# Performance work log

Hardware: AMD Instinct MI355X
Metric: run time of the kernel (lower is better)

Reference implementation:

```python
import jax, jax.numpy as jnp
import numpy as np


def setup_inputs() -> dict:
    key = jax.random.key(0)
    k1, k2 = jax.random.split(key)
    pred_corners = jax.random.normal(k1, (2048, 8, 3), dtype=jnp.float32)
    gt_corners = jax.random.normal(k2, (2048, 8, 3), dtype=jnp.float32)
    return {"pred_corners": pred_corners, "gt_corners": gt_corners}


def _chamfer(pred_corners, gt_corners):
    # flatten boxes -> point clouds: [Np*8, 3], [Ng*8, 3]
    x = pred_corners.reshape(-1, 3)
    y = gt_corners.reshape(-1, 3)
    x2 = jnp.sum(x * x, axis=-1)  # [N]
    y2 = jnp.sum(y * y, axis=-1)  # [M]
    d2 = x2[:, None] + y2[None, :] - 2.0 * jnp.einsum("nd,md->nm", x, y)
    dist = jnp.sqrt(jnp.maximum(d2, 0.0))  # [N, M]
    # bidirectional min, averaged per box (8 corners) then over boxes
    min_p2g = jnp.min(dist, axis=1).reshape(-1, 8).mean(axis=1)
    min_g2p = jnp.min(dist, axis=0).reshape(-1, 8).mean(axis=1)
    return min_p2g.mean() + min_g2p.mean()


def reference(pred_corners, gt_corners):
    return _chamfer(pred_corners, gt_corners)
```

## Files before the change

### kernel.cpp

```cpp
#include <hip/hip_runtime.h>


#define NPTS   16384
#define BLOCK  256
#define XW     128
#define XCH    512
#define NXB    (NPTS / XCH)
#define YRNG   1024
#define NYR    (NPTS / YRNG)
#define CHT    8
#define NCH    (YRNG / (CHT * 16))
#define ONEBF  0x3F80

#define WS_PPB  (1u << 20)
#define WS_PGA  (2u << 20)
#define WS_PGB  (3u << 20)
#define WS_PART (4u << 20)

typedef __attribute__((ext_vector_type(8))) short bf16x8;
typedef __attribute__((ext_vector_type(4))) float f32x4;
typedef __attribute__((ext_vector_type(4))) unsigned int u32x4;

__device__ inline unsigned short f2bf(float f) {
    unsigned int u = __float_as_uint(f);
    return (unsigned short)((u + 0x7FFFu + ((u >> 16) & 1u)) >> 16);
}
__device__ inline float bf2f(unsigned short h) {
    return __uint_as_float((unsigned int)h << 16);
}
__device__ inline void split3(float v, unsigned short* s) {
    unsigned short h = f2bf(v);  float r = v - bf2f(h);
    unsigned short m = f2bf(r);  r -= bf2f(m);
    s[0] = h; s[1] = m; s[2] = f2bf(r);
}

__device__ inline void build_rows(const float p[3], unsigned short* a,
                                  unsigned short* b) {
    const int CI[6] = {0, 0, 1, 0, 1, 2};
    const int CJ[6] = {0, 1, 0, 2, 1, 0};
    unsigned short xs[3][3], nn[3], t[3];
#pragma unroll
    for (int d = 0; d < 3; ++d) {
        split3(p[d], t);
        xs[0][d] = t[0]; xs[1][d] = t[1]; xs[2][d] = t[2];
    }
    split3(-0.5f * (p[0]*p[0] + p[1]*p[1] + p[2]*p[2]), nn);
#pragma unroll
    for (int c = 0; c < 6; ++c)
#pragma unroll
        for (int d = 0; d < 3; ++d) {
            a[c*3+d] = xs[CI[c]][d];
            b[c*3+d] = xs[CJ[c]][d];
        }
#pragma unroll
    for (int k = 0; k < 3; ++k) {
        a[18+k] = nn[k];  b[18+k] = ONEBF;
        a[21+k] = ONEBF;  b[21+k] = nn[k];
    }
#pragma unroll
    for (int k = 24; k < 32; ++k) { a[k] = 0; b[k] = 0; }
}

__device__ inline void store_row_swz(uint4* dst4, int i, const unsigned short* s) {
    unsigned int w[16];
#pragma unroll
    for (int k = 0; k < 16; ++k)
        w[k] = (unsigned int)s[2*k] | ((unsigned int)s[2*k+1] << 16);
    const int base = (i >> 4) * 64 + (i & 15);
#pragma unroll
    for (int kgc = 0; kgc < 4; ++kgc)
        dst4[base + kgc * 16] = make_uint4(w[4*kgc], w[4*kgc+1],
                                           w[4*kgc+2], w[4*kgc+3]);
}

__global__ __launch_bounds__(256) void pack_points(
        const float* __restrict__ pred, const float* __restrict__ gt,
        unsigned short* __restrict__ Ppa, unsigned short* __restrict__ Ppb,
        unsigned short* __restrict__ Pga, unsigned short* __restrict__ Pgb,
        float* __restrict__ out) {
    const int i = blockIdx.x * 256 + threadIdx.x;
    if (i == 0) out[0] = 0.0f;
    if (i >= NPTS) return;
    float p[3] = {pred[3*i], pred[3*i+1], pred[3*i+2]};
    float q[3] = {gt[3*i],   gt[3*i+1],   gt[3*i+2]};
    unsigned short ra[32], rb[32];
    build_rows(p, ra, rb);
    store_row_swz(reinterpret_cast<uint4*>(Ppa), i, ra);
    store_row_swz(reinterpret_cast<uint4*>(Ppb), i, rb);
    build_rows(q, ra, rb);
    store_row_swz(reinterpret_cast<uint4*>(Pga), i, ra);
    store_row_swz(reinterpret_cast<uint4*>(Pgb), i, rb);
}

template <int CTRL>
__device__ inline float rormax(float v) {
    int t = __builtin_amdgcn_update_dpp(0, __float_as_int(v), CTRL, 0xF, 0xF,
                                        false);
    return fmaxf(v, __int_as_float(t));
}

__global__ __launch_bounds__(BLOCK, 1) void chamfer_rowmin(
        const unsigned short* __restrict__ Ppa,
        const unsigned short* __restrict__ Ppb,
        const unsigned short* __restrict__ Pga,
        const unsigned short* __restrict__ Pgb,
        float* __restrict__ part) {
    const int xb  = blockIdx.x;
    const int yr  = blockIdx.y;
    const int dir = blockIdx.z;
    const unsigned short* __restrict__ Ap = dir ? Pga : Ppa;
    const unsigned short* __restrict__ Bp = dir ? Ppb : Pgb;
    const int tid = threadIdx.x;
    const int lane = tid & 63, w = tid >> 6;
    const int col = lane & 15, kg = lane >> 4;
    const int frag = kg * 16 + col;

    __shared__ uint4 buf[2][CHT * 64];
    __shared__ float rowacc[XCH];

    const uint4* ap = reinterpret_cast<const uint4*>(Ap);
    const int tile0 = xb * 32 + w * 8;
    u32x4 af[8];
#pragma unroll
    for (int xi = 0; xi < 8; ++xi)
        af[xi] = *reinterpret_cast<const u32x4*>(&ap[(tile0 + xi) * 64 + frag]);

    f32x4 rmax[8];
#pragma unroll
    for (int xi = 0; xi < 8; ++xi)
        rmax[xi] = (f32x4){-3.0e38f, -3.0e38f, -3.0e38f, -3.0e38f};

    const u32x4 zz = {0u, 0u, 0u, 0u};

    const uint4* bp = reinterpret_cast<const uint4*>(Bp) + (size_t)(yr * 64) * 64;
    uint4 s0 = bp[tid];
    uint4 s1 = bp[256 + tid];

#pragma unroll 1
    for (int c = 0; c < NCH; ++c) {
        buf[c & 1][tid]       = s0;
        buf[c & 1][256 + tid] = s1;
        __syncthreads();
        if (c + 1 < NCH) {
            s0 = bp[(c + 1) * 512 + tid];
            s1 = bp[(c + 1) * 512 + 256 + tid];
        }
        const uint4* bb = buf[c & 1];
#pragma unroll
        for (int t = 0; t < CHT; t += 2) {
            u32x4 c0 = *reinterpret_cast<const u32x4*>(&bb[(t + 0) * 64 + frag]);
            u32x4 c1 = *reinterpret_cast<const u32x4*>(&bb[(t + 1) * 64 + frag]);
#pragma unroll
            for (int xi = 0; xi < 8; ++xi) {
                f32x4 A, B;
                asm("s_nop 1\n\t"
                    "v_mfma_f32_16x16x32_bf16 %0, %2, %3, %5\n\t"
                    "v_mfma_f32_16x16x32_bf16 %1, %2, %4, %5\n\t"
                    "s_nop 7\n\t"
                    "s_nop 7\n\t"
                    "s_nop 3"
                    : "=&v"(A), "=&v"(B)
                    : "v"(af[xi]), "v"(c0), "v"(c1), "v"(zz));
                rmax[xi].x = fmaxf(fmaxf(A.x, B.x), rmax[xi].x);
                rmax[xi].y = fmaxf(fmaxf(A.y, B.y), rmax[xi].y);
                rmax[xi].z = fmaxf(fmaxf(A.z, B.z), rmax[xi].z);
                rmax[xi].w = fmaxf(fmaxf(A.w, B.w), rmax[xi].w);
            }
        }
        __syncthreads();
    }

#pragma unroll
    for (int xi = 0; xi < 8; ++xi) {
#pragma unroll
        for (int cc = 0; cc < 4; ++cc) {
            float v = rmax[xi][cc];
            v = rormax<0x121>(v);
            v = rormax<0x122>(v);
            v = rormax<0x124>(v);
            v = rormax<0x128>(v);
            if (col == 0)
                rowacc[w * XW + xi * 16 + kg * 4 + cc] = fmaxf(-2.0f * v, 0.0f);
        }
    }
    __syncthreads();
    float* dst = part + (size_t)(dir * NYR + yr) * NPTS + xb * XCH;
    dst[tid]       = rowacc[tid];
    dst[256 + tid] = rowacc[256 + tid];
}

__global__ __launch_bounds__(256) void chamfer_reduce(
        const float* __restrict__ part, float* __restrict__ out) {
    const int gid = blockIdx.x * 256 + threadIdx.x;
    const int side = gid >> 12;
    const int idx4 = (gid & 4095) * 4;
    const float* base = part + (size_t)side * NYR * NPTS + idx4;
    float4 m = make_float4(3.0e38f, 3.0e38f, 3.0e38f, 3.0e38f);
#pragma unroll
    for (int c = 0; c < NYR; ++c) {
        float4 v = *reinterpret_cast<const float4*>(base + (size_t)c * NPTS);
        m.x = fminf(m.x, v.x); m.y = fminf(m.y, v.y);
        m.z = fminf(m.z, v.z); m.w = fminf(m.w, v.w);
    }
    float s = sqrtf(m.x) + sqrtf(m.y) + sqrtf(m.z) + sqrtf(m.w);
#pragma unroll
    for (int o = 32; o > 0; o >>= 1)
        s += __shfl_down(s, o, 64);
    if ((threadIdx.x & 63) == 0)
        atomicAdd(out, s * (1.0f / (float)NPTS));
}

extern "C" void kernel_launch(void* const* d_in, const int* in_sizes, int n_in,
                              void* d_out, int out_size, void* d_ws, size_t ws_size,
                              hipStream_t stream) {
    const float* pred = (const float*)d_in[0];
    const float* gt   = (const float*)d_in[1];
    float* out        = (float*)d_out;
    unsigned short* Ppa = (unsigned short*)d_ws;
    unsigned short* Ppb = (unsigned short*)((char*)d_ws + WS_PPB);
    unsigned short* Pga = (unsigned short*)((char*)d_ws + WS_PGA);
    unsigned short* Pgb = (unsigned short*)((char*)d_ws + WS_PGB);
    float* part         = (float*)((char*)d_ws + WS_PART);

    hipLaunchKernelGGL(pack_points, dim3(NPTS / 256), dim3(256), 0, stream,
                       pred, gt, Ppa, Ppb, Pga, Pgb, out);
    hipLaunchKernelGGL(chamfer_rowmin, dim3(NXB, NYR, 2), dim3(BLOCK), 0, stream,
                       Ppa, Ppb, Pga, Pgb, part);
    hipLaunchKernelGGL(chamfer_reduce, dim3(2 * NPTS / 1024), dim3(256), 0, stream,
                       part, out);
}
```

Measured before the change: 90.13 us.

## Compute both chamfer directions from one distance matrix pass

Replaces the two-direction launch, which computed the pred-to-gt and gt-to-pred matrices separately, with one kernel that computes each distance tile once. Row minima come from the existing per-row max path, and column minima are built by reducing across the MFMA output and lanes into shared memory. This roughly halves the MFMA work and packs only two of the four operand arrays. The y-range per block is cut to 512 to keep the grid large, and the hand-scheduled inline asm with its s_nop padding is replaced by compiler builtins. The cost is extra fmax and shuffle work per tile, plus more shared memory and partial-result traffic per block.

```diff
diff --git a/kernel.cpp b/kernel.cpp
--- a/kernel.cpp
+++ b/kernel.cpp
@@ -6,20 +6,19 @@
 #define XW     128
 #define XCH    512
 #define NXB    (NPTS / XCH)
-#define YRNG   1024
+#define YRNG   512
 #define NYR    (NPTS / YRNG)
 #define CHT    8
 #define NCH    (YRNG / (CHT * 16))
 #define ONEBF  0x3F80
 
-#define WS_PPB  (1u << 20)
-#define WS_PGA  (2u << 20)
-#define WS_PGB  (3u << 20)
-#define WS_PART (4u << 20)
+#define WS_PGB  (1u << 20)
+#define WS_PART (2u << 20)
+#define NROWSL  NYR
+#define NCOLSL  NXB
 
 typedef __attribute__((ext_vector_type(8))) short bf16x8;
 typedef __attribute__((ext_vector_type(4))) float f32x4;
-typedef __attribute__((ext_vector_type(4))) unsigned int u32x4;
 
 __device__ inline unsigned short f2bf(float f) {
     unsigned int u = __float_as_uint(f);
@@ -75,8 +74,7 @@
 
 __global__ __launch_bounds__(256) void pack_points(
         const float* __restrict__ pred, const float* __restrict__ gt,
-        unsigned short* __restrict__ Ppa, unsigned short* __restrict__ Ppb,
-        unsigned short* __restrict__ Pga, unsigned short* __restrict__ Pgb,
+        unsigned short* __restrict__ Ppa, unsigned short* __restrict__ Pgb,
         float* __restrict__ out) {
     const int i = blockIdx.x * 256 + threadIdx.x;
     if (i == 0) out[0] = 0.0f;
@@ -86,9 +84,7 @@
     unsigned short ra[32], rb[32];
     build_rows(p, ra, rb);
     store_row_swz(reinterpret_cast<uint4*>(Ppa), i, ra);
-    store_row_swz(reinterpret_cast<uint4*>(Ppb), i, rb);
     build_rows(q, ra, rb);
-    store_row_swz(reinterpret_cast<uint4*>(Pga), i, ra);
     store_row_swz(reinterpret_cast<uint4*>(Pgb), i, rb);
 }
 
@@ -99,17 +95,12 @@
     return fmaxf(v, __int_as_float(t));
 }
 
-__global__ __launch_bounds__(BLOCK, 1) void chamfer_rowmin(
+__global__ __launch_bounds__(BLOCK, 1) void chamfer_bidi(
         const unsigned short* __restrict__ Ppa,
-        const unsigned short* __restrict__ Ppb,
-        const unsigned short* __restrict__ Pga,
         const unsigned short* __restrict__ Pgb,
         float* __restrict__ part) {
-    const int xb  = blockIdx.x;
-    const int yr  = blockIdx.y;
-    const int dir = blockIdx.z;
-    const unsigned short* __restrict__ Ap = dir ? Pga : Ppa;
-    const unsigned short* __restrict__ Bp = dir ? Ppb : Pgb;
+    const int yr = blockIdx.x;
+    const int xb = blockIdx.y;
     const int tid = threadIdx.x;
     const int lane = tid & 63, w = tid >> 6;
     const int col = lane & 15, kg = lane >> 4;
@@ -117,22 +108,26 @@
 
     __shared__ uint4 buf[2][CHT * 64];
     __shared__ float rowacc[XCH];
-
-    const uint4* ap = reinterpret_cast<const uint4*>(Ap);
+    __shared__ float colacc[4][YRNG];
+
+    const uint4* ap = reinterpret_cast<const uint4*>(Ppa);
     const int tile0 = xb * 32 + w * 8;
-    u32x4 af[8];
+    bf16x8 af[8];
 #pragma unroll
     for (int xi = 0; xi < 8; ++xi)
-        af[xi] = *reinterpret_cast<const u32x4*>(&ap[(tile0 + xi) * 64 + frag]);
+        af[xi] = *reinterpret_cast<const bf16x8*>(&ap[(tile0 + xi) * 64 + frag]);
 
     f32x4 rmax[8];
 #pragma unroll
     for (int xi = 0; xi < 8; ++xi)
         rmax[xi] = (f32x4){-3.0e38f, -3.0e38f, -3.0e38f, -3.0e38f};
-
-    const u32x4 zz = {0u, 0u, 0u, 0u};
-
-    const uint4* bp = reinterpret_cast<const uint4*>(Bp) + (size_t)(yr * 64) * 64;
+    float cmax[CHT];
+#pragma unroll
+    for (int yt = 0; yt < CHT; ++yt) cmax[yt] = -3.0e38f;
+
+    const f32x4 z4 = {0.0f, 0.0f, 0.0f, 0.0f};
+
+    const uint4* bp = reinterpret_cast<const uint4*>(Pgb) + (size_t)yr * 2048;
     uint4 s0 = bp[tid];
     uint4 s1 = bp[256 + tid];
 
@@ -148,24 +143,29 @@
         const uint4* bb = buf[c & 1];
 #pragma unroll
         for (int t = 0; t < CHT; t += 2) {
-            u32x4 c0 = *reinterpret_cast<const u32x4*>(&bb[(t + 0) * 64 + frag]);
-            u32x4 c1 = *reinterpret_cast<const u32x4*>(&bb[(t + 1) * 64 + frag]);
+            bf16x8 b0 = *reinterpret_cast<const bf16x8*>(&bb[(t + 0) * 64 + frag]);
+            bf16x8 b1 = *reinterpret_cast<const bf16x8*>(&bb[(t + 1) * 64 + frag]);
 #pragma unroll
             for (int xi = 0; xi < 8; ++xi) {
-                f32x4 A, B;
-                asm("s_nop 1\n\t"
-                    "v_mfma_f32_16x16x32_bf16 %0, %2, %3, %5\n\t"
-                    "v_mfma_f32_16x16x32_bf16 %1, %2, %4, %5\n\t"
-                    "s_nop 7\n\t"
-                    "s_nop 7\n\t"
-                    "s_nop 3"
-                    : "=&v"(A), "=&v"(B)
-                    : "v"(af[xi]), "v"(c0), "v"(c1), "v"(zz));
+                f32x4 A = __builtin_amdgcn_mfma_f32_16x16x32_bf16(af[xi], b0, z4, 0, 0, 0);
+                f32x4 B = __builtin_amdgcn_mfma_f32_16x16x32_bf16(af[xi], b1, z4, 0, 0, 0);
                 rmax[xi].x = fmaxf(fmaxf(A.x, B.x), rmax[xi].x);
                 rmax[xi].y = fmaxf(fmaxf(A.y, B.y), rmax[xi].y);
                 rmax[xi].z = fmaxf(fmaxf(A.z, B.z), rmax[xi].z);
                 rmax[xi].w = fmaxf(fmaxf(A.w, B.w), rmax[xi].w);
+                float ta = fmaxf(fmaxf(A.x, A.y), A.z);
+                cmax[t]     = fmaxf(fmaxf(ta, A.w), cmax[t]);
+                float tb = fmaxf(fmaxf(B.x, B.y), B.z);
+                cmax[t + 1] = fmaxf(fmaxf(tb, B.w), cmax[t + 1]);
             }
+        }
+#pragma unroll
+        for (int yt = 0; yt < CHT; ++yt) {
+            float v = cmax[yt];
+            v = fmaxf(v, __shfl_xor(v, 16, 64));
+            v = fmaxf(v, __shfl_xor(v, 32, 64));
+            if (kg == 0) colacc[w][c * 128 + yt * 16 + col] = v;
+            cmax[yt] = -3.0e38f;
         }
         __syncthreads();
     }
@@ -184,9 +184,18 @@
         }
     }
     __syncthreads();
-    float* dst = part + (size_t)(dir * NYR + yr) * NPTS + xb * XCH;
-    dst[tid]       = rowacc[tid];
-    dst[256 + tid] = rowacc[256 + tid];
+
+    float* rdst = part + (size_t)yr * NPTS + xb * XCH;
+    rdst[tid]       = rowacc[tid];
+    rdst[256 + tid] = rowacc[256 + tid];
+    float* cdst = part + (size_t)(NROWSL + xb) * NPTS + yr * YRNG;
+#pragma unroll
+    for (int j = 0; j < 2; ++j) {
+        int idx = j * 256 + tid;
+        float v = fmaxf(fmaxf(colacc[0][idx], colacc[1][idx]),
+                        fmaxf(colacc[2][idx], colacc[3][idx]));
+        cdst[idx] = fmaxf(-2.0f * v, 0.0f);
+    }
 }
 
 __global__ __launch_bounds__(256) void chamfer_reduce(
@@ -194,10 +203,10 @@
     const int gid = blockIdx.x * 256 + threadIdx.x;
     const int side = gid >> 12;
     const int idx4 = (gid & 4095) * 4;
-    const float* base = part + (size_t)side * NYR * NPTS + idx4;
+    const float* base = part + (size_t)side * NROWSL * NPTS + idx4;
     float4 m = make_float4(3.0e38f, 3.0e38f, 3.0e38f, 3.0e38f);
 #pragma unroll
-    for (int c = 0; c < NYR; ++c) {
+    for (int c = 0; c < 32; ++c) {
         float4 v = *reinterpret_cast<const float4*>(base + (size_t)c * NPTS);
         m.x = fminf(m.x, v.x); m.y = fminf(m.y, v.y);
         m.z = fminf(m.z, v.z); m.w = fminf(m.w, v.w);
@@ -217,15 +226,13 @@
     const float* gt   = (const float*)d_in[1];
     float* out        = (float*)d_out;
     unsigned short* Ppa = (unsigned short*)d_ws;
-    unsigned short* Ppb = (unsigned short*)((char*)d_ws + WS_PPB);
-    unsigned short* Pga = (unsigned short*)((char*)d_ws + WS_PGA);
     unsigned short* Pgb = (unsigned short*)((char*)d_ws + WS_PGB);
     float* part         = (float*)((char*)d_ws + WS_PART);
 
     hipLaunchKernelGGL(pack_points, dim3(NPTS / 256), dim3(256), 0, stream,
-                       pred, gt, Ppa, Ppb, Pga, Pgb, out);
-    hipLaunchKernelGGL(chamfer_rowmin, dim3(NXB, NYR, 2), dim3(BLOCK), 0, stream,
-                       Ppa, Ppb, Pga, Pgb, part);
+                       pred, gt, Ppa, Pgb, out);
+    hipLaunchKernelGGL(chamfer_bidi, dim3(NYR, NXB), dim3(BLOCK), 0, stream,
+                       Ppa, Pgb, part);
     hipLaunchKernelGGL(chamfer_reduce, dim3(2 * NPTS / 1024), dim3(256), 0, stream,
                        part, out);
 }
```

New measurement: 192.0 us. +113.0%, slower.
